# Kernel optimization log

Hardware: AMD Instinct MI355X
Metric: run time of the kernel (lower is better)

## Reference

```python
import jax, jax.numpy as jnp
import numpy as np

B, L, D, H = 16, 1024, 1024, 16
HD = D // H  # head dim = 64


def setup_inputs() -> dict:
    rng = jax.random.key(0)
    ks = jax.random.split(rng, 12)
    s = 0.02
    return {
        "key": jax.random.normal(ks[0], (B, L, D), jnp.float32),
        "value": jax.random.normal(ks[1], (B, L, D), jnp.float32),
        "query": jax.random.normal(ks[2], (B, L, D), jnp.float32),
        "atten_masks": jax.random.randint(ks[3], (B, L, L), 0, 2, jnp.int32),
        "Wk": jax.random.normal(ks[4], (D, D), jnp.float32) * s,
        "bk": jnp.zeros((D,), jnp.float32),
        "Wq": jax.random.normal(ks[5], (D, D), jnp.float32) * s,
        "bq": jnp.zeros((D,), jnp.float32),
        "Wv": jax.random.normal(ks[6], (D, D), jnp.float32) * s,
        "bv": jnp.zeros((D,), jnp.float32),
        "Wp": jax.random.normal(ks[7], (D, D), jnp.float32) * s,
        "bp": jnp.zeros((D,), jnp.float32),
    }


def reference(key, value, query, atten_masks, Wk, bk, Wq, bq, Wv, bv, Wp, bp):
    # Linear projections (torch nn.Linear: x @ W^T + b)
    def lin(x, W, b):
        return x @ W.T + b

    # [B, L, D] -> [B, H, L, HD]
    def heads(x):
        return x.reshape(B, L, H, HD).transpose(0, 2, 1, 3)

    k = heads(lin(key, Wk, bk))
    q = heads(lin(query, Wq, bq))
    v = heads(lin(value, Wv, bv))

    scale = 1.0 / np.sqrt(HD).astype(np.float32)
    att = jnp.einsum("bhqd,bhkd->bhqk", q, k) * scale  # [B, H, L, L]
    att = jnp.where(atten_masks[:, None, :, :] == 0, -jnp.inf, att)
    att = jax.nn.softmax(att, axis=-1)

    y = jnp.einsum("bhqk,bhkd->bhqd", att, v)  # [B, H, L, HD]
    y = y.transpose(0, 2, 1, 3).reshape(B, L, D)
    return lin(y, Wp, bp)
```

## Files before the change

### kernel.cpp

```cpp
#include <hip/hip_runtime.h>

typedef __bf16 bf16_t;
typedef __bf16 bf16x4 __attribute__((ext_vector_type(4)));
typedef __bf16 bf16x8 __attribute__((ext_vector_type(8)));
typedef float f32x4 __attribute__((ext_vector_type(4)));
typedef float f32x16 __attribute__((ext_vector_type(16)));

__device__ __forceinline__ int swz(int row) { return (row ^ (row >> 3)) & 7; }
__device__ __forceinline__ int swz2(int row) { return (row ^ (row >> 2)) & 3; }

__device__ __forceinline__ f32x4 mfma16(bf16x8 a, bf16x8 b, f32x4 c) {
  return __builtin_amdgcn_mfma_f32_16x16x32_bf16(a, b, c, 0, 0, 0);
}
__device__ __forceinline__ f32x16 mfma32(bf16x8 a, bf16x8 b, f32x16 c) {
  return __builtin_amdgcn_mfma_f32_32x32x16_bf16(a, b, c, 0, 0, 0);
}

__device__ __forceinline__ void gl_lds16(const void* g, void* l) {
  __builtin_amdgcn_global_load_lds(
      (const __attribute__((address_space(1))) unsigned int*)g,
      (__attribute__((address_space(3))) unsigned int*)l, 16, 0, 0);
}

__global__ __launch_bounds__(256) void cvtw_kernel(const float* __restrict__ s,
                                                   bf16_t* __restrict__ d) {
  int i = blockIdx.x * 256 + threadIdx.x;
  float4 v = ((const float4*)s)[i];
  bf16x4 o;
  o[0] = (bf16_t)v.x; o[1] = (bf16_t)v.y; o[2] = (bf16_t)v.z; o[3] = (bf16_t)v.w;
  ((bf16x4*)d)[i] = o;
}

__global__ __launch_bounds__(256) void pack_mask_kernel(
    const int* __restrict__ mask, unsigned* __restrict__ bits) {
  int idx = blockIdx.x * 256 + threadIdx.x;
  const int4* src = (const int4*)(mask + (size_t)idx * 32);
  unsigned w = 0;
#pragma unroll
  for (int i = 0; i < 8; ++i) {
    int4 v = src[i];
    w |= (v.x != 0 ? 1u : 0u) << (i * 4 + 0);
    w |= (v.y != 0 ? 1u : 0u) << (i * 4 + 1);
    w |= (v.z != 0 ? 1u : 0u) << (i * 4 + 2);
    w |= (v.w != 0 ? 1u : 0u) << (i * 4 + 3);
  }
  bits[idx] = w;
}

template <typename AT, typename OT>
__device__ __forceinline__ void gemm256_body(const AT* __restrict__ A,
                                             const bf16_t* __restrict__ W,
                                             const float* __restrict__ bias,
                                             OT* __restrict__ O) {
  __shared__ __align__(16) bf16_t As[2][256 * 32];
  __shared__ __align__(16) bf16_t Bs[2][256 * 32];

  const int t = threadIdx.x;
  const int lane = t & 63;
  const int wid = t >> 6;
  const int g = lane >> 4;
  const int lr = lane & 15;
  const int wm = wid >> 2, wn = wid & 3;
  const int lid = blockIdx.x;
  const int logical = (lid & 7) * 32 + (lid >> 3);
  const int m0 = (logical >> 2) * 256;
  const int n0 = (logical & 3) * 256;

  const int row0 = t >> 2, c0 = t & 3;
  const int row1 = 128 + row0;

  f32x4 acc[8][4] = {};
  f32x4 fa0[2], fa1[2];

  auto LOAD = [&](int buf, int kb) {
    if constexpr (sizeof(AT) == 4) {
      const float* p0 = (const float*)A + (size_t)(m0 + row0) * 1024 + kb + c0 * 8;
      const float* p1 = (const float*)A + (size_t)(m0 + row1) * 1024 + kb + c0 * 8;
      fa0[0] = *(const f32x4*)p0;
      fa0[1] = *(const f32x4*)(p0 + 4);
      fa1[0] = *(const f32x4*)p1;
      fa1[1] = *(const f32x4*)(p1 + 4);
    } else {
#pragma unroll
      for (int rr = 0; rr < 2; ++rr) {
        int s = rr * 512 + t;
        int row = s >> 2, c = s & 3;
        gl_lds16((const bf16_t*)A + (size_t)(m0 + row) * 1024 + kb + (c ^ swz2(row)) * 8,
                 &As[buf][(rr * 512 + wid * 64) * 8]);
      }
    }
#pragma unroll
    for (int rr = 0; rr < 2; ++rr) {
      int s = rr * 512 + t;
      int row = s >> 2, c = s & 3;
      gl_lds16(W + (size_t)(n0 + row) * 1024 + kb + (c ^ swz2(row)) * 8,
               &Bs[buf][(rr * 512 + wid * 64) * 8]);
    }
  };

  auto WRITEA = [&](int buf) {
    if constexpr (sizeof(AT) == 4) {
      bf16x8 v0, v1;
#pragma unroll
      for (int e = 0; e < 4; ++e) {
        v0[e] = (bf16_t)fa0[0][e];
        v0[e + 4] = (bf16_t)fa0[1][e];
        v1[e] = (bf16_t)fa1[0][e];
        v1[e + 4] = (bf16_t)fa1[1][e];
      }
      *(bf16x8*)&As[buf][row0 * 32 + ((c0 ^ swz2(row0))) * 8] = v0;
      *(bf16x8*)&As[buf][row1 * 32 + ((c0 ^ swz2(row1))) * 8] = v1;
    }
  };

  LOAD(0, 0);
  WRITEA(0);
  __syncthreads();
  int cur = 0;

  for (int kb = 0; kb < 1024; kb += 32) {
    const bool more = kb < 992;
    if (more) LOAD(cur ^ 1, kb + 32);

    bf16x8 a[8], b[4];
#pragma unroll
    for (int i = 0; i < 8; ++i) {
      int row = wm * 128 + i * 16 + lr;
      a[i] = *(const bf16x8*)&As[cur][row * 32 + ((g ^ swz2(row))) * 8];
    }
#pragma unroll
    for (int j = 0; j < 4; ++j) {
      int row = wn * 64 + j * 16 + lr;
      b[j] = *(const bf16x8*)&Bs[cur][row * 32 + ((g ^ swz2(row))) * 8];
    }
    __builtin_amdgcn_s_setprio(1);
#pragma unroll
    for (int i = 0; i < 8; ++i)
#pragma unroll
      for (int j = 0; j < 4; ++j)
        acc[i][j] = mfma16(a[i], b[j], acc[i][j]);
    __builtin_amdgcn_s_setprio(0);

    if (more) WRITEA(cur ^ 1);
    __syncthreads();
    cur ^= 1;
  }

  float bval[4];
#pragma unroll
  for (int j = 0; j < 4; ++j) bval[j] = bias[n0 + wn * 64 + j * 16 + lr];
#pragma unroll
  for (int i = 0; i < 8; ++i)
#pragma unroll
    for (int r = 0; r < 4; ++r) {
      int row = m0 + wm * 128 + i * 16 + g * 4 + r;
#pragma unroll
      for (int j = 0; j < 4; ++j) {
        int n = n0 + wn * 64 + j * 16 + lr;
        O[(size_t)row * 1024 + n] = (OT)(acc[i][j][r] + bval[j]);
      }
    }
}

__global__ __launch_bounds__(512, 2) void gemm256_qkv_f32_kernel(
    const float* key, const float* query, const float* value,
    const bf16_t* Wkb, const bf16_t* Wqb, const bf16_t* Wvb, const float* bk,
    const float* bq, const float* bv, bf16_t* ko, bf16_t* qo, bf16_t* vo) {
  const float *A, *bi;
  const bf16_t* W;
  bf16_t* O;
  if (blockIdx.y == 0) { A = key; W = Wkb; bi = bk; O = ko; }
  else if (blockIdx.y == 1) { A = query; W = Wqb; bi = bq; O = qo; }
  else { A = value; W = Wvb; bi = bv; O = vo; }
  gemm256_body<float, bf16_t>(A, W, bi, O);
}

__global__ __launch_bounds__(512, 2) void gemm256_out_kernel(
    const bf16_t* __restrict__ A, const bf16_t* __restrict__ W,
    const float* __restrict__ b, float* __restrict__ O) {
  gemm256_body<bf16_t, float>(A, W, b, O);
}

__global__ __launch_bounds__(256) void transpose_v_kernel(
    const bf16_t* __restrict__ v_ws, bf16_t* __restrict__ vT) {
  __shared__ bf16_t T[64 * 66];
  const int kc = blockIdx.x, h = blockIdx.y, b = blockIdx.z;
  const int t = threadIdx.x;
  {
    int key = t >> 2, dblk = t & 3;
    const bf16_t* src =
        v_ws + ((size_t)(b * 1024 + kc * 64 + key)) * 1024 + h * 64 + dblk * 16;
    bf16x8 a0 = *(const bf16x8*)src;
    bf16x8 a1 = *(const bf16x8*)(src + 8);
    bf16_t* row = &T[key * 66 + dblk * 16];
#pragma unroll
    for (int j = 0; j < 4; ++j) {
      ((unsigned*)row)[j] = ((const unsigned*)&a0)[j];
      ((unsigned*)row)[j + 4] = ((const unsigned*)&a1)[j];
    }
  }
  __syncthreads();
  {
    int d = t >> 2, kcl = t & 3;
    bf16x8 o0, o1;
#pragma unroll
    for (int e = 0; e < 8; ++e) {
      o0[e] = T[(kcl * 16 + e) * 66 + d];
      o1[e] = T[(kcl * 16 + 8 + e) * 66 + d];
    }
    bf16_t* dst =
        vT + ((size_t)((b * 16 + h) * 64 + d)) * 1024 + kc * 64 + kcl * 16;
    *(bf16x8*)dst = o0;
    *(bf16x8*)(dst + 8) = o1;
  }
}

#define ATTN_M2 10.0f

__global__ __launch_bounds__(256) void attn_kernel(
    const bf16_t* __restrict__ q_ws, const bf16_t* __restrict__ k_ws,
    const bf16_t* __restrict__ vT, const unsigned* __restrict__ mbits,
    bf16_t* __restrict__ y_ws) {
  __shared__ __align__(16) bf16_t Ks[64 * 64];
  __shared__ __align__(16) bf16_t Vs[64 * 64];
  __shared__ __align__(16) bf16_t Ps[4][32 * 64];

  const int lid = blockIdx.x;
  const int logical = (lid & 7) * 256 + (lid >> 3);
  const int qb = logical & 7;
  const int h = (logical >> 3) & 15;
  const int b = logical >> 7;
  const int t = threadIdx.x, lane = t & 63, wid = t >> 6;
  const int ql = lane & 31;
  const int hh = lane >> 5;
  const int q = qb * 128 + wid * 32 + ql;

  bf16x8 qf[4];
  {
    const bf16_t* qp = q_ws + ((size_t)(b * 1024 + q)) * 1024 + h * 64 + hh * 8;
#pragma unroll
    for (int kc = 0; kc < 4; ++kc) {
      bf16x8 raw = *(const bf16x8*)(qp + kc * 16);
      bf16x8 sc;
#pragma unroll
      for (int e = 0; e < 8; ++e)
        sc[e] = (bf16_t)((float)raw[e] * 0.18033688f);
      qf[kc] = sc;
    }
  }

  float l = 0.f;
  f32x16 acc0 = {}, acc1 = {};
  const bf16_t* Kb = k_ws + ((size_t)b * 1024) * 1024 + h * 64;
  const bf16_t* Vb = vT + ((size_t)((b * 16 + h) * 64)) * 1024;
  const unsigned* mrow = mbits + ((size_t)(b * 1024 + q)) * 32;

  for (int kb = 0; kb < 16; ++kb) {
    __syncthreads();
#pragma unroll
    for (int rr = 0; rr < 2; ++rr) {
      int s = rr * 256 + t;
      int row = s >> 3, c = s & 7;
      gl_lds16(Kb + (size_t)(kb * 64 + row) * 1024 + (c ^ swz(row)) * 8,
               &Ks[(rr * 256 + wid * 64) * 8]);
      gl_lds16(Vb + (size_t)row * 1024 + kb * 64 + (c ^ swz(row)) * 8,
               &Vs[(rr * 256 + wid * 64) * 8]);
    }
    uint2 mw = *(const uint2*)&mrow[kb * 2];
    __syncthreads();

    f32x16 c0 = {}, c1 = {};
    __builtin_amdgcn_s_setprio(1);
#pragma unroll
    for (int kc = 0; kc < 4; ++kc) {
      int sl = kc * 2 + hh;
      {
        int row = ql;
        bf16x8 kf = *(const bf16x8*)&Ks[row * 64 + ((sl ^ swz(row))) * 8];
        c0 = mfma32(kf, qf[kc], c0);
      }
      {
        int row = 32 + ql;
        bf16x8 kf = *(const bf16x8*)&Ks[row * 64 + ((sl ^ swz(row))) * 8];
        c1 = mfma32(kf, qf[kc], c1);
      }
    }
    __builtin_amdgcn_s_setprio(0);

    unsigned wx = mw.x >> (4 * hh);
    unsigned wy = mw.y >> (4 * hh);
    float p0[16], p1[16];
    float ps = 0.f;
#pragma unroll
    for (int r = 0; r < 16; ++r) {
      const int posr = (r & 3) + 8 * (r >> 2);
      int n0m = (int)(wx << (31 - posr)) >> 31;
      int n1m = (int)(wy << (31 - posr)) >> 31;
      float e0 = __builtin_amdgcn_exp2f(c0[r] - ATTN_M2);
      float e1 = __builtin_amdgcn_exp2f(c1[r] - ATTN_M2);
      e0 = __int_as_float(__float_as_int(e0) & n0m);
      e1 = __int_as_float(__float_as_int(e1) & n1m);
      p0[r] = e0;
      p1[r] = e1;
      ps += e0 + e1;
    }
    ps += __shfl_xor(ps, 32);
    l += ps;

#pragma unroll
    for (int j = 0; j < 4; ++j) {
      bf16x4 w0, w1;
#pragma unroll
      for (int e = 0; e < 4; ++e) {
        w0[e] = (bf16_t)p0[4 * j + e];
        w1[e] = (bf16_t)p1[4 * j + e];
      }
      int off = 4 * hh;
      *(bf16x4*)&Ps[wid][ql * 64 + ((j ^ swz(ql)) * 8) + off] = w0;
      *(bf16x4*)&Ps[wid][ql * 64 + (((4 + j) ^ swz(ql)) * 8) + off] = w1;
    }
    bf16x8 pb[4];
#pragma unroll
    for (int kc = 0; kc < 4; ++kc) {
      int sl = kc * 2 + hh;
      pb[kc] = *(const bf16x8*)&Ps[wid][ql * 64 + ((sl ^ swz(ql))) * 8];
    }

    __builtin_amdgcn_s_setprio(1);
#pragma unroll
    for (int kc = 0; kc < 4; ++kc) {
      int sl = kc * 2 + hh;
      {
        int row = ql;
        bf16x8 vf = *(const bf16x8*)&Vs[row * 64 + ((sl ^ swz(row))) * 8];
        acc0 = mfma32(vf, pb[kc], acc0);
      }
      {
        int row = 32 + ql;
        bf16x8 vf = *(const bf16x8*)&Vs[row * 64 + ((sl ^ swz(row))) * 8];
        acc1 = mfma32(vf, pb[kc], acc1);
      }
    }
    __builtin_amdgcn_s_setprio(0);
  }

  float inv = 1.0f / fmaxf(l, 1e-30f);
  bf16_t* yp = y_ws + ((size_t)(b * 1024 + q)) * 1024 + h * 64;
#pragma unroll
  for (int j = 0; j < 4; ++j) {
    bf16x4 o0, o1;
#pragma unroll
    for (int e = 0; e < 4; ++e) {
      o0[e] = (bf16_t)(acc0[4 * j + e] * inv);
      o1[e] = (bf16_t)(acc1[4 * j + e] * inv);
    }
    *(bf16x4*)&yp[8 * j + 4 * hh] = o0;
    *(bf16x4*)&yp[32 + 8 * j + 4 * hh] = o1;
  }
}

extern "C" void kernel_launch(void* const* d_in, const int* in_sizes, int n_in,
                              void* d_out, int out_size, void* d_ws,
                              size_t ws_size, hipStream_t stream) {
  (void)in_sizes; (void)n_in; (void)out_size; (void)ws_size;
  const float* key = (const float*)d_in[0];
  const float* value = (const float*)d_in[1];
  const float* query = (const float*)d_in[2];
  const int* mask = (const int*)d_in[3];
  const float* Wk = (const float*)d_in[4];
  const float* bk = (const float*)d_in[5];
  const float* Wq = (const float*)d_in[6];
  const float* bq = (const float*)d_in[7];
  const float* Wv = (const float*)d_in[8];
  const float* bv = (const float*)d_in[9];
  const float* Wp = (const float*)d_in[10];
  const float* bp = (const float*)d_in[11];
  float* out = (float*)d_out;

  char* ws = (char*)d_ws;
  const size_t MB = 1ull << 20;
  unsigned* mbits = (unsigned*)(ws);
  bf16_t* Wkb = (bf16_t*)(ws + 2 * MB);
  bf16_t* Wqb = (bf16_t*)(ws + 4 * MB);
  bf16_t* Wvb = (bf16_t*)(ws + 6 * MB);
  bf16_t* Wpb = (bf16_t*)(ws + 8 * MB);
  bf16_t* k_ws = (bf16_t*)(ws + 10 * MB);
  bf16_t* q_ws = (bf16_t*)(ws + 42 * MB);
  bf16_t* v_ws = (bf16_t*)(ws + 74 * MB);
  bf16_t* y_ws = (bf16_t*)(ws + 106 * MB);
  bf16_t* vT_ws = (bf16_t*)(ws + 138 * MB);

  cvtw_kernel<<<1024, 256, 0, stream>>>(Wk, Wkb);
  cvtw_kernel<<<1024, 256, 0, stream>>>(Wq, Wqb);
  cvtw_kernel<<<1024, 256, 0, stream>>>(Wv, Wvb);
  cvtw_kernel<<<1024, 256, 0, stream>>>(Wp, Wpb);
  pack_mask_kernel<<<2048, 256, 0, stream>>>(mask, mbits);

  gemm256_qkv_f32_kernel<<<dim3(256, 3), 512, 0, stream>>>(
      key, query, value, Wkb, Wqb, Wvb, bk, bq, bv, k_ws, q_ws, v_ws);
  transpose_v_kernel<<<dim3(16, 16, 16), 256, 0, stream>>>(v_ws, vT_ws);
  attn_kernel<<<2048, 256, 0, stream>>>(q_ws, k_ws, vT_ws, mbits, y_ws);
  gemm256_out_kernel<<<256, 512, 0, stream>>>(y_ws, Wpb, bp, out);
}
```

Before: 401.0 us.

## Pre-convert fp32 activations to bf16 in one fused conversion kernel

All fp32 inputs (key, query, value and the four weights) and the mask packing now go through a single conversion kernel that writes bf16 copies, replacing five separate small launches. The QKV GEMM then reads bf16 activations through direct global-to-LDS async loads instead of loading fp32 into registers and converting before writing to LDS. This shortens the GEMM's inner pipeline and cuts launch overhead, at the cost of an extra full read and write pass over the 3x64MB activations. Workspace buffers are reassigned so the bf16 input buffers are reused for vT and y.

```diff
diff --git a/kernel.cpp b/kernel.cpp
--- a/kernel.cpp
+++ b/kernel.cpp
@@ -22,33 +22,50 @@
       (__attribute__((address_space(3))) unsigned int*)l, 16, 0, 0);
 }
 
-__global__ __launch_bounds__(256) void cvtw_kernel(const float* __restrict__ s,
-                                                   bf16_t* __restrict__ d) {
-  int i = blockIdx.x * 256 + threadIdx.x;
+__global__ __launch_bounds__(256) void cvt_all_kernel(
+    const float* __restrict__ key, const float* __restrict__ query,
+    const float* __restrict__ value, const float* __restrict__ Wk,
+    const float* __restrict__ Wq, const float* __restrict__ Wv,
+    const float* __restrict__ Wp, const int* __restrict__ mask,
+    bf16_t* __restrict__ I1, bf16_t* __restrict__ I2, bf16_t* __restrict__ I3,
+    bf16_t* __restrict__ Wkb, bf16_t* __restrict__ Wqb,
+    bf16_t* __restrict__ Wvb, bf16_t* __restrict__ Wpb,
+    unsigned* __restrict__ mbits) {
+  const int bid = blockIdx.x;
+  if (bid >= 53248) {
+    int idx = (bid - 53248) * 256 + threadIdx.x;
+    const int4* src = (const int4*)(mask + (size_t)idx * 32);
+    unsigned w = 0;
+#pragma unroll
+    for (int i = 0; i < 8; ++i) {
+      int4 v = src[i];
+      w |= (v.x != 0 ? 1u : 0u) << (i * 4 + 0);
+      w |= (v.y != 0 ? 1u : 0u) << (i * 4 + 1);
+      w |= (v.z != 0 ? 1u : 0u) << (i * 4 + 2);
+      w |= (v.w != 0 ? 1u : 0u) << (i * 4 + 3);
+    }
+    mbits[idx] = w;
+    return;
+  }
+  const float* s;
+  bf16_t* d;
+  int base;
+  if (bid < 16384) { s = key; d = I1; base = bid; }
+  else if (bid < 32768) { s = query; d = I2; base = bid - 16384; }
+  else if (bid < 49152) { s = value; d = I3; base = bid - 32768; }
+  else if (bid < 50176) { s = Wk; d = Wkb; base = bid - 49152; }
+  else if (bid < 51200) { s = Wq; d = Wqb; base = bid - 50176; }
+  else if (bid < 52224) { s = Wv; d = Wvb; base = bid - 51200; }
+  else { s = Wp; d = Wpb; base = bid - 52224; }
+  int i = base * 256 + threadIdx.x;
   float4 v = ((const float4*)s)[i];
   bf16x4 o;
   o[0] = (bf16_t)v.x; o[1] = (bf16_t)v.y; o[2] = (bf16_t)v.z; o[3] = (bf16_t)v.w;
   ((bf16x4*)d)[i] = o;
 }
 
-__global__ __launch_bounds__(256) void pack_mask_kernel(
-    const int* __restrict__ mask, unsigned* __restrict__ bits) {
-  int idx = blockIdx.x * 256 + threadIdx.x;
-  const int4* src = (const int4*)(mask + (size_t)idx * 32);
-  unsigned w = 0;
-#pragma unroll
-  for (int i = 0; i < 8; ++i) {
-    int4 v = src[i];
-    w |= (v.x != 0 ? 1u : 0u) << (i * 4 + 0);
-    w |= (v.y != 0 ? 1u : 0u) << (i * 4 + 1);
-    w |= (v.z != 0 ? 1u : 0u) << (i * 4 + 2);
-    w |= (v.w != 0 ? 1u : 0u) << (i * 4 + 3);
-  }
-  bits[idx] = w;
-}
-
-template <typename AT, typename OT>
-__device__ __forceinline__ void gemm256_body(const AT* __restrict__ A,
+template <typename OT>
+__device__ __forceinline__ void gemm256_body(const bf16_t* __restrict__ A,
                                              const bf16_t* __restrict__ W,
                                              const float* __restrict__ bias,
                                              OT* __restrict__ O) {
@@ -66,61 +83,26 @@
   const int m0 = (logical >> 2) * 256;
   const int n0 = (logical & 3) * 256;
 
-  const int row0 = t >> 2, c0 = t & 3;
-  const int row1 = 128 + row0;
-
   f32x4 acc[8][4] = {};
-  f32x4 fa0[2], fa1[2];
-
-  auto LOAD = [&](int buf, int kb) {
-    if constexpr (sizeof(AT) == 4) {
-      const float* p0 = (const float*)A + (size_t)(m0 + row0) * 1024 + kb + c0 * 8;
-      const float* p1 = (const float*)A + (size_t)(m0 + row1) * 1024 + kb + c0 * 8;
-      fa0[0] = *(const f32x4*)p0;
-      fa0[1] = *(const f32x4*)(p0 + 4);
-      fa1[0] = *(const f32x4*)p1;
-      fa1[1] = *(const f32x4*)(p1 + 4);
-    } else {
-#pragma unroll
-      for (int rr = 0; rr < 2; ++rr) {
-        int s = rr * 512 + t;
-        int row = s >> 2, c = s & 3;
-        gl_lds16((const bf16_t*)A + (size_t)(m0 + row) * 1024 + kb + (c ^ swz2(row)) * 8,
-                 &As[buf][(rr * 512 + wid * 64) * 8]);
-      }
-    }
+
+  auto STAGE = [&](int buf, int kb) {
 #pragma unroll
     for (int rr = 0; rr < 2; ++rr) {
       int s = rr * 512 + t;
       int row = s >> 2, c = s & 3;
+      gl_lds16(A + (size_t)(m0 + row) * 1024 + kb + (c ^ swz2(row)) * 8,
+               &As[buf][(rr * 512 + wid * 64) * 8]);
       gl_lds16(W + (size_t)(n0 + row) * 1024 + kb + (c ^ swz2(row)) * 8,
                &Bs[buf][(rr * 512 + wid * 64) * 8]);
     }
   };
 
-  auto WRITEA = [&](int buf) {
-    if constexpr (sizeof(AT) == 4) {
-      bf16x8 v0, v1;
-#pragma unroll
-      for (int e = 0; e < 4; ++e) {
-        v0[e] = (bf16_t)fa0[0][e];
-        v0[e + 4] = (bf16_t)fa0[1][e];
-        v1[e] = (bf16_t)fa1[0][e];
-        v1[e + 4] = (bf16_t)fa1[1][e];
-      }
-      *(bf16x8*)&As[buf][row0 * 32 + ((c0 ^ swz2(row0))) * 8] = v0;
-      *(bf16x8*)&As[buf][row1 * 32 + ((c0 ^ swz2(row1))) * 8] = v1;
-    }
-  };
-
-  LOAD(0, 0);
-  WRITEA(0);
+  STAGE(0, 0);
   __syncthreads();
   int cur = 0;
 
   for (int kb = 0; kb < 1024; kb += 32) {
-    const bool more = kb < 992;
-    if (more) LOAD(cur ^ 1, kb + 32);
+    if (kb < 992) STAGE(cur ^ 1, kb + 32);
 
     bf16x8 a[8], b[4];
 #pragma unroll
@@ -141,7 +123,6 @@
         acc[i][j] = mfma16(a[i], b[j], acc[i][j]);
     __builtin_amdgcn_s_setprio(0);
 
-    if (more) WRITEA(cur ^ 1);
     __syncthreads();
     cur ^= 1;
   }
@@ -162,23 +143,23 @@
     }
 }
 
-__global__ __launch_bounds__(512, 2) void gemm256_qkv_f32_kernel(
-    const float* key, const float* query, const float* value,
+__global__ __launch_bounds__(512, 2) void gemm256_qkv_kernel(
+    const bf16_t* key, const bf16_t* query, const bf16_t* value,
     const bf16_t* Wkb, const bf16_t* Wqb, const bf16_t* Wvb, const float* bk,
     const float* bq, const float* bv, bf16_t* ko, bf16_t* qo, bf16_t* vo) {
-  const float *A, *bi;
-  const bf16_t* W;
+  const bf16_t *A, *W;
+  const float* bi;
   bf16_t* O;
   if (blockIdx.y == 0) { A = key; W = Wkb; bi = bk; O = ko; }
   else if (blockIdx.y == 1) { A = query; W = Wqb; bi = bq; O = qo; }
   else { A = value; W = Wvb; bi = bv; O = vo; }
-  gemm256_body<float, bf16_t>(A, W, bi, O);
+  gemm256_body<bf16_t>(A, W, bi, O);
 }
 
 __global__ __launch_bounds__(512, 2) void gemm256_out_kernel(
     const bf16_t* __restrict__ A, const bf16_t* __restrict__ W,
     const float* __restrict__ b, float* __restrict__ O) {
-  gemm256_body<bf16_t, float>(A, W, b, O);
+  gemm256_body<float>(A, W, b, O);
 }
 
 __global__ __launch_bounds__(256) void transpose_v_kernel(
@@ -384,20 +365,20 @@
   bf16_t* Wqb = (bf16_t*)(ws + 4 * MB);
   bf16_t* Wvb = (bf16_t*)(ws + 6 * MB);
   bf16_t* Wpb = (bf16_t*)(ws + 8 * MB);
-  bf16_t* k_ws = (bf16_t*)(ws + 10 * MB);
-  bf16_t* q_ws = (bf16_t*)(ws + 42 * MB);
-  bf16_t* v_ws = (bf16_t*)(ws + 74 * MB);
-  bf16_t* y_ws = (bf16_t*)(ws + 106 * MB);
-  bf16_t* vT_ws = (bf16_t*)(ws + 138 * MB);
-
-  cvtw_kernel<<<1024, 256, 0, stream>>>(Wk, Wkb);
-  cvtw_kernel<<<1024, 256, 0, stream>>>(Wq, Wqb);
-  cvtw_kernel<<<1024, 256, 0, stream>>>(Wv, Wvb);
-  cvtw_kernel<<<1024, 256, 0, stream>>>(Wp, Wpb);
-  pack_mask_kernel<<<2048, 256, 0, stream>>>(mask, mbits);
-
-  gemm256_qkv_f32_kernel<<<dim3(256, 3), 512, 0, stream>>>(
-      key, query, value, Wkb, Wqb, Wvb, bk, bq, bv, k_ws, q_ws, v_ws);
+  bf16_t* I1 = (bf16_t*)(ws + 10 * MB);
+  bf16_t* I2 = (bf16_t*)(ws + 42 * MB);
+  bf16_t* I3 = (bf16_t*)(ws + 74 * MB);
+  bf16_t* k_ws = (bf16_t*)(ws + 106 * MB);
+  bf16_t* q_ws = (bf16_t*)(ws + 138 * MB);
+  bf16_t* v_ws = (bf16_t*)(ws + 170 * MB);
+  bf16_t* vT_ws = I1;
+  bf16_t* y_ws = I2;
+
+  cvt_all_kernel<<<55296, 256, 0, stream>>>(key, query, value, Wk, Wq, Wv, Wp,
+                                            mask, I1, I2, I3, Wkb, Wqb, Wvb,
+                                            Wpb, mbits);
+  gemm256_qkv_kernel<<<dim3(256, 3), 512, 0, stream>>>(
+      I1, I2, I3, Wkb, Wqb, Wvb, bk, bq, bv, k_ws, q_ws, v_ws);
   transpose_v_kernel<<<dim3(16, 16, 16), 256, 0, stream>>>(v_ws, vT_ws);
   attn_kernel<<<2048, 256, 0, stream>>>(q_ws, k_ws, vT_ws, mbits, y_ws);
   gemm256_out_kernel<<<256, 512, 0, stream>>>(y_ws, Wpb, bp, out);
```

After: 374.1 us. 6.7% less time.
